# Performance work log

Measured on AMD Instinct MI355X. Metric: run time of the kernel, lower is better.

The kernel has to match this reference:

```python
import jax, jax.numpy as jnp
import numpy as np

N_NODES = 50000
N_REL = 8
D_IN = 64      # review_dim (in_feats)
D_OUT = 32     # attention_feats (final_dim)
H = 2          # num_heads
N_EDGES = 800000
NEG_SLOPE = 0.2


def gather_mm(x, w, b, idx):
    """Per-edge relation-indexed GEMM: out[e] = x[e] @ w[idx[e]] + b[idx[e]].
    Loops over the small fixed relation set (R=8) instead of materializing
    an [E, D, HF] gathered weight tensor."""
    out = jnp.zeros((x.shape[0], w.shape[-1]), dtype=x.dtype)
    for r in range(w.shape[0]):
        out = out + jnp.where((idx == r)[:, None], x @ w[r] + b[r], jnp.zeros((), x.dtype))
    return out


def setup_inputs() -> dict:
    key = jax.random.key(0)
    ks = jax.random.split(key, 11)
    feat = jax.random.normal(ks[0], (N_NODES, D_IN), dtype=jnp.float32)
    src = jax.random.randint(ks[1], (N_EDGES,), 0, N_NODES)
    dst = jax.random.randint(ks[2], (N_EDGES,), 0, N_NODES)
    r_type = jax.random.randint(ks[3], (N_EDGES,), 0, N_REL)
    nid = jax.random.randint(ks[4], (N_EDGES,), 0, N_NODES)
    fc_src = jax.random.normal(ks[5], (N_REL, D_IN, H * D_OUT), dtype=jnp.float32) * 0.1
    fc_src_bias = jax.random.normal(ks[6], (N_REL, H * D_OUT), dtype=jnp.float32) * 0.1
    node_quality = jax.random.normal(ks[7], (N_NODES, D_IN), dtype=jnp.float32)
    fc_qual = jax.random.normal(ks[8], (N_REL, D_IN, H * D_OUT), dtype=jnp.float32) * 0.1
    fc_qual_bias = jax.random.normal(ks[9], (N_REL, H * D_OUT), dtype=jnp.float32) * 0.1
    attn = jax.random.normal(ks[10], (N_REL, H, D_OUT), dtype=jnp.float32) * 0.1
    return {"feat": feat, "src": src, "dst": dst, "r_type": r_type, "nid": nid,
            "fc_src": fc_src, "fc_src_bias": fc_src_bias, "node_quality": node_quality,
            "fc_qual": fc_qual, "fc_qual_bias": fc_qual_bias, "attn": attn}


def reference(feat, src, dst, r_type, nid, fc_src, fc_src_bias,
              node_quality, fc_qual, fc_qual_bias, attn):
    E = src.shape[0]
    h_src = feat  # feat_drop is identity (p=0)

    # el: relation-aware projection of source features, per edge -> [E, H, D_OUT]
    el = gather_mm(h_src[src], fc_src, fc_src_bias, r_type).reshape(E, H, D_OUT)
    # qual: relation-aware projection of per-edge node-quality embedding
    h_qual = node_quality[nid]
    qual = gather_mm(h_qual, fc_qual, fc_qual_bias, r_type).reshape(E, H, D_OUT)

    # additive attention logits, relation-indexed attn vector -> [E, H]
    e = jax.nn.leaky_relu(el + qual, negative_slope=NEG_SLOPE)
    e = jnp.sum(e * attn[r_type], axis=-1)  # [E, H]

    # edge_softmax over incoming edges of each dst node (per head)
    emax = jax.ops.segment_max(e, dst, num_segments=N_NODES)  # [N, H]
    emax = jnp.where(jnp.isfinite(emax), emax, jnp.zeros((), e.dtype))
    ex = jnp.exp(e - emax[dst])
    denom = jax.ops.segment_sum(ex, dst, num_segments=N_NODES)
    a = ex / denom[dst]  # [E, H]

    # NARRE: messages are raw source features weighted by attention
    msg = h_src[src][:, None, :] * a[:, :, None]  # [E, H, D_IN]
    rst = jax.ops.segment_sum(msg, dst, num_segments=N_NODES)  # [N, H, D_IN]
    return rst
```

## Files before the change

kernel.cpp:

```cpp
#include <hip/hip_runtime.h>
#include <hip/hip_bf16.h>

#define NN 50000
#define NR 8
#define NE 800000
#define NBLK_E 3125
#define NWV (NBLK_E * 4)
#define NCH 13

typedef short bf16x8 __attribute__((ext_vector_type(8)));
typedef float f32x4  __attribute__((ext_vector_type(4)));

__device__ __forceinline__ unsigned fkey(float f) {
    unsigned b = __float_as_uint(f);
    return (b & 0x80000000u) ? ~b : (b | 0x80000000u);
}
__device__ __forceinline__ float funkey(unsigned k) {
    unsigned b = (k & 0x80000000u) ? (k ^ 0x80000000u) : ~k;
    return __uint_as_float(b);
}
__device__ __forceinline__ unsigned short f2bf(float f) {
    unsigned u = __float_as_uint(f);
    unsigned r = (u + 0x7FFFu + ((u >> 16) & 1u)) >> 16;
    return (unsigned short)r;
}
__device__ __forceinline__ float bf2f(unsigned short b) {
    return __uint_as_float(((unsigned)b) << 16);
}

__global__ __launch_bounds__(256) void conv_hist_kernel(
    const float* __restrict__ feat, const float* __restrict__ nq,
    const float* __restrict__ WS, const float* __restrict__ WQ,
    const float* __restrict__ bS, const float* __restrict__ bQ,
    const int* __restrict__ dst, const int* __restrict__ rt,
    unsigned short* __restrict__ xS, unsigned short* __restrict__ xQ,
    unsigned short* __restrict__ WtS, unsigned short* __restrict__ WtQ,
    float* __restrict__ bSQ,
    int* __restrict__ cnt, int* __restrict__ rank, int* __restrict__ rhist)
{
    const int t = threadIdx.x;
    const int idx = blockIdx.x * 256 + t;

    if (blockIdx.x < 2 * NBLK_E && (blockIdx.x & 1) == 0) {
        const int eb = blockIdx.x >> 1;
        const int e = eb * 256 + t;
        const int w = t >> 6, lane = t & 63;
        const int d = dst[e], r = rt[e];
        rank[e] = atomicAdd(&cnt[d], 1);
        #pragma unroll
        for (int rr = 0; rr < 8; ++rr) {
            const unsigned long long m = __ballot(r == rr);
            if (lane == 0) rhist[rr * NWV + eb * 4 + w] = __popcll(m);
        }
    }

    const int NX = NN * 64 / 4;
    if (idx < NX) {
        const float4 v = reinterpret_cast<const float4*>(feat)[idx];
        ushort4 p; p.x = f2bf(v.x); p.y = f2bf(v.y); p.z = f2bf(v.z); p.w = f2bf(v.w);
        reinterpret_cast<ushort4*>(xS)[idx] = p;
    } else if (idx < 2 * NX) {
        const float4 v = reinterpret_cast<const float4*>(nq)[idx - NX];
        ushort4 p; p.x = f2bf(v.x); p.y = f2bf(v.y); p.z = f2bf(v.z); p.w = f2bf(v.w);
        reinterpret_cast<ushort4*>(xQ)[idx - NX] = p;
    } else {
        int i = idx - 2 * NX;
        if (i < 32768) {
            const int r = i >> 12, rem = i & 4095, o = rem >> 6, k = rem & 63;
            WtS[i] = f2bf(WS[(size_t)r * 4096 + k * 64 + o]);
        } else if (i < 65536) {
            i -= 32768;
            const int r = i >> 12, rem = i & 4095, o = rem >> 6, k = rem & 63;
            WtQ[i] = f2bf(WQ[(size_t)r * 4096 + k * 64 + o]);
        } else if (i < 65536 + 512) {
            const int j = i - 65536;
            bSQ[j] = bS[j] + bQ[j];
        }
    }
}

__global__ __launch_bounds__(256) void scanrb1_kernel(
    const int* __restrict__ rhist, int* __restrict__ rbase0, int* __restrict__ psum)
{
    __shared__ int s[256];
    __shared__ int carry;
    const int c = blockIdx.x, r = blockIdx.y, t = threadIdx.x;
    if (t == 0) carry = 0;
    __syncthreads();
    const int i1 = min((c + 1) * 1024, NWV);
    for (int b0 = c * 1024; b0 < i1; b0 += 256) {
        const int i = b0 + t;
        const int v = (i < i1) ? rhist[r * NWV + i] : 0;
        s[t] = v;
        __syncthreads();
        #pragma unroll
        for (int off = 1; off < 256; off <<= 1) {
            const int x = (t >= off) ? s[t - off] : 0;
            __syncthreads();
            s[t] += x;
            __syncthreads();
        }
        if (i < i1) rbase0[r * NWV + i] = carry + s[t] - v;
        __syncthreads();
        if (t == 0) carry += s[255];
        __syncthreads();
    }
    if (t == 0) psum[r * NCH + c] = carry;
}

__global__ __launch_bounds__(256) void scan1_kernel(
    const int* __restrict__ cnt, int* __restrict__ offs, int* __restrict__ partial)
{
    __shared__ int s[256];
    const int t = threadIdx.x, i = blockIdx.x * 256 + t;
    const int v = (i < NN) ? cnt[i] : 0;
    s[t] = v;
    __syncthreads();
    #pragma unroll
    for (int off = 1; off < 256; off <<= 1) {
        const int x = (t >= off) ? s[t - off] : 0;
        __syncthreads();
        s[t] += x;
        __syncthreads();
    }
    if (i < NN) offs[i] = s[t] - v;
    if (t == 255) partial[blockIdx.x] = s[255];
}

__global__ __launch_bounds__(256) void scan2_kernel(
    int* __restrict__ partial, const int nblk,
    const int* __restrict__ psum, int* __restrict__ off_pad,
    int* __restrict__ cbase, int4* __restrict__ meta)
{
    __shared__ int s[256];
    __shared__ int sop[9];
    __shared__ int scr[8];
    const int t = threadIdx.x;
    const int v = (t < nblk) ? partial[t] : 0;
    s[t] = v;
    __syncthreads();
    #pragma unroll
    for (int off = 1; off < 256; off <<= 1) {
        const int x = (t >= off) ? s[t - off] : 0;
        __syncthreads();
        s[t] += x;
        __syncthreads();
    }
    if (t < nblk) partial[t] = s[t] - v;
    if (t == 0) {
        int cr[8];
        for (int r = 0; r < NR; ++r) {
            cr[r] = 0;
            for (int c = 0; c < NCH; ++c) cr[r] += psum[r * NCH + c];
        }
        int acc = 0;
        for (int r = 0; r < NR; ++r) {
            sop[r] = acc; off_pad[r] = acc; scr[r] = cr[r];
            int a2 = acc;
            for (int c = 0; c < NCH; ++c) { cbase[r * NCH + c] = a2; a2 += psum[r * NCH + c]; }
            acc += (cr[r] + 255) & ~255;
        }
        sop[8] = acc; off_pad[8] = acc;
    }
    __syncthreads();
    for (int r = 0; r < NR; ++r) {
        const int s0 = sop[r] + scr[r], s1 = sop[r + 1];
        for (int i = s0 + t; i < s1; i += 256) meta[i] = make_int4(0, 0, -1, 0);
    }
}

__global__ __launch_bounds__(256) void scan3_kernel(
    int* __restrict__ offs, const int* __restrict__ partial)
{
    const int i = blockIdx.x * 256 + threadIdx.x;
    if (i < NN) offs[i] += partial[blockIdx.x];
    if (i == 0) offs[NN] = NE;
}

__global__ __launch_bounds__(256) void fillr_kernel(
    const int* __restrict__ rt, const int* __restrict__ src,
    const int* __restrict__ nid, const int* __restrict__ dst,
    const int* __restrict__ offs, const int* __restrict__ rank,
    const int* __restrict__ rbase0, const int* __restrict__ cbase,
    int4* __restrict__ meta)
{
    const int t = threadIdx.x, e = blockIdx.x * 256 + t;
    const int w = t >> 6, lane = t & 63;
    const int r = rt[e];
    unsigned long long mymask = 0;
    #pragma unroll
    for (int rr = 0; rr < 8; ++rr) {
        const unsigned long long m = __ballot(r == rr);
        if (r == rr) mymask = m;
    }
    const int rk = (int)__popcll(mymask & ((1ull << lane) - 1ull));
    const int wv = blockIdx.x * 4 + w;
    const int slot = cbase[r * NCH + (wv >> 10)] + rbase0[r * NWV + wv] + rk;
    const int j = offs[dst[e]] + rank[e];
    meta[slot] = make_int4(src[e], nid[e], j, 0);
}

__global__ __launch_bounds__(256) void logits_kernel(
    const unsigned short* __restrict__ xS, const unsigned short* __restrict__ xQ,
    const unsigned short* __restrict__ WtS, const unsigned short* __restrict__ WtQ,
    const float* __restrict__ bSQ, const float* __restrict__ attn,
    const int4* __restrict__ meta, const int* __restrict__ off_pad,
    uint2* __restrict__ perm)
{
    __shared__ bf16x8 ldsS[512];
    __shared__ bf16x8 ldsQ[512];
    const int slot0 = blockIdx.x * 256;
    int r = 0;
    #pragma unroll
    for (int i = 1; i <= 8; ++i) r += (slot0 >= off_pad[i]);
    if (r >= 8) return;

    const int t = threadIdx.x;
    const int lane = t & 63, l15 = lane & 15, g = lane >> 4, l7 = l15 & 7;
    const int sbase = slot0 + (t >> 6) * 64;

    int4 mt[4];
    #pragma unroll
    for (int b = 0; b < 4; ++b) mt[b] = meta[sbase + b * 16 + l15];
    bf16x8 xf[4][2], qf[4][2];
    #pragma unroll
    for (int b = 0; b < 4; ++b) {
        const unsigned short* xp = xS + (size_t)mt[b].x * 64;
        const unsigned short* qp = xQ + (size_t)mt[b].y * 64;
        xf[b][0] = *reinterpret_cast<const bf16x8*>(xp + g * 8);
        xf[b][1] = *reinterpret_cast<const bf16x8*>(xp + 32 + g * 8);
        qf[b][0] = *reinterpret_cast<const bf16x8*>(qp + g * 8);
        qf[b][1] = *reinterpret_cast<const bf16x8*>(qp + 32 + g * 8);
    }

    #pragma unroll
    for (int i = 0; i < 2; ++i) {
        const int c = t + i * 256;
        const int row = c >> 3, c8 = c & 7, sw = c8 ^ (row & 7);
        ldsS[row * 8 + sw] = *reinterpret_cast<const bf16x8*>(WtS + (size_t)r * 4096 + c * 8);
        ldsQ[row * 8 + sw] = *reinterpret_cast<const bf16x8*>(WtQ + (size_t)r * 4096 + c * 8);
    }
    __syncthreads();

    float p0[4] = {0.f, 0.f, 0.f, 0.f}, p1[4] = {0.f, 0.f, 0.f, 0.f};
    #pragma unroll
    for (int ot = 0; ot < 4; ++ot) {
        const int row8 = (ot * 16 + l15) * 8;
        const bf16x8 wS0 = ldsS[row8 + (g ^ l7)];
        const bf16x8 wS1 = ldsS[row8 + ((4 + g) ^ l7)];
        const bf16x8 wQ0 = ldsQ[row8 + (g ^ l7)];
        const bf16x8 wQ1 = ldsQ[row8 + ((4 + g) ^ l7)];
        const f32x4 bv = *reinterpret_cast<const f32x4*>(bSQ  + r * 64 + ot * 16 + g * 4);
        const f32x4 av = *reinterpret_cast<const f32x4*>(attn + r * 64 + ot * 16 + g * 4);
        #pragma unroll
        for (int b = 0; b < 4; ++b) {
            f32x4 acc = (f32x4){0.f, 0.f, 0.f, 0.f};
            acc = __builtin_amdgcn_mfma_f32_16x16x32_bf16(wS0, xf[b][0], acc, 0, 0, 0);
            acc = __builtin_amdgcn_mfma_f32_16x16x32_bf16(wS1, xf[b][1], acc, 0, 0, 0);
            acc = __builtin_amdgcn_mfma_f32_16x16x32_bf16(wQ0, qf[b][0], acc, 0, 0, 0);
            acc = __builtin_amdgcn_mfma_f32_16x16x32_bf16(wQ1, qf[b][1], acc, 0, 0, 0);
            float part = 0.f;
            #pragma unroll
            for (int j = 0; j < 4; ++j) {
                float v = acc[j] + bv[j];
                v = v > 0.f ? v : 0.2f * v;
                part += v * av[j];
            }
            if (ot < 2) p0[b] += part; else p1[b] += part;
        }
    }
    #pragma unroll
    for (int b = 0; b < 4; ++b) {
        p0[b] += __shfl_xor(p0[b], 16); p0[b] += __shfl_xor(p0[b], 32);
        p1[b] += __shfl_xor(p1[b], 16); p1[b] += __shfl_xor(p1[b], 32);
        if (g == 0 && mt[b].z >= 0) {
            const unsigned pk = ((unsigned)f2bf(p0[b]) << 16) | (unsigned)f2bf(p1[b]);
            perm[mt[b].z] = make_uint2((unsigned)mt[b].x, pk);
        }
    }
}

__global__ __launch_bounds__(256) void aggregate_kernel(
    const unsigned short* __restrict__ xS, const int* __restrict__ offs,
    const uint2* __restrict__ perm, float* __restrict__ out)
{
    __shared__ float2 ebuf[4][64];
    __shared__ int    sbuf[4][64];
    const int wv = threadIdx.x >> 6;
    const int n = blockIdx.x * 4 + wv;
    if (n >= NN) return;
    const int lane = threadIdx.x & 63;
    const int h2 = lane >> 5;
    const int dp = lane & 31;
    const int s0 = offs[n], s1 = offs[n + 1];
    float a00 = 0.f, a01 = 0.f, a10 = 0.f, a11 = 0.f;
    float d0s = 0.f, d1s = 0.f;
    if (s1 > s0) {
        float m0 = -1e30f, m1 = -1e30f;
        for (int j = s0 + lane; j < s1; j += 64) {
            const uint2 p = perm[j];
            m0 = fmaxf(m0, bf2f((unsigned short)(p.y >> 16)));
            m1 = fmaxf(m1, bf2f((unsigned short)(p.y & 0xFFFFu)));
        }
        #pragma unroll
        for (int m = 32; m; m >>= 1) {
            m0 = fmaxf(m0, __shfl_xor(m0, m));
            m1 = fmaxf(m1, __shfl_xor(m1, m));
        }
        for (int c = s0; c < s1; c += 64) {
            const int cnt = min(64, s1 - c);
            if (lane < cnt) {
                const uint2 p = perm[c + lane];
                const float e0 = __expf(bf2f((unsigned short)(p.y >> 16)) - m0);
                const float e1 = __expf(bf2f((unsigned short)(p.y & 0xFFFFu)) - m1);
                d0s += e0; d1s += e1;
                ebuf[wv][lane] = make_float2(e0, e1);
                sbuf[wv][lane] = (int)p.x;
            } else if (lane == cnt) {
                ebuf[wv][lane] = make_float2(0.f, 0.f);
                sbuf[wv][lane] = 0;
            }
            const int cp = cnt + (cnt & 1);
            #pragma unroll 4
            for (int k = 0; k < cp; k += 2) {
                const int ei = k + h2;
                const int sA = sbuf[wv][ei];
                const float2 w = ebuf[wv][ei];
                const unsigned fv = *reinterpret_cast<const unsigned*>(
                    xS + (size_t)sA * 64 + dp * 2);
                const float fx = bf2f((unsigned short)(fv & 0xFFFFu));
                const float fy = bf2f((unsigned short)(fv >> 16));
                a00 += fx * w.x; a01 += fy * w.x;
                a10 += fx * w.y; a11 += fy * w.y;
            }
        }
        #pragma unroll
        for (int m = 32; m; m >>= 1) {
            d0s += __shfl_xor(d0s, m);
            d1s += __shfl_xor(d1s, m);
        }
        a00 += __shfl_xor(a00, 32); a01 += __shfl_xor(a01, 32);
        a10 += __shfl_xor(a10, 32); a11 += __shfl_xor(a11, 32);
        const float r0 = 1.f / d0s, r1 = 1.f / d1s;
        a00 *= r0; a01 *= r0; a10 *= r1; a11 *= r1;
    }
    if (h2 == 0)
        *reinterpret_cast<float2*>(&out[(size_t)n * 128 + dp * 2])      = make_float2(a00, a01);
    else
        *reinterpret_cast<float2*>(&out[(size_t)n * 128 + 64 + dp * 2]) = make_float2(a10, a11);
}

__global__ __launch_bounds__(256) void logits_direct_kernel(
    const float* __restrict__ feat, const float* __restrict__ nq,
    const int* __restrict__ src, const int* __restrict__ dst,
    const int* __restrict__ rt, const int* __restrict__ nid,
    const float* __restrict__ fc_src, const float* __restrict__ fc_src_b,
    const float* __restrict__ fc_qual, const float* __restrict__ fc_qual_b,
    const float* __restrict__ attn,
    float* __restrict__ e_buf, unsigned* __restrict__ emax)
{
    __shared__ float Ws[64][64];
    __shared__ float Wq[64][64];
    __shared__ float bl[64];
    __shared__ float al[64];
    const int r = blockIdx.y;
    const int t = threadIdx.x;
    for (int i = t; i < 4096; i += 256) {
        ((float*)Ws)[i] = fc_src[(size_t)r * 4096 + i];
        ((float*)Wq)[i] = fc_qual[(size_t)r * 4096 + i];
    }
    if (t < 64) {
        bl[t] = fc_src_b[r * 64 + t] + fc_qual_b[r * 64 + t];
        al[t] = attn[r * 64 + t];
    }
    __syncthreads();

    const int lane = t & 63;
    const int wid = blockIdx.x * 4 + (t >> 6);
    const int nw = gridDim.x * 4;
    for (int e = wid; e < NE; e += nw) {
        if (rt[e] != r) continue;
        const int s = src[e], q = nid[e];
        float fv = feat[(size_t)s * 64 + lane];
        float qv = nq[(size_t)q * 64 + lane];
        float acc = bl[lane];
        for (int k = 0; k < 64; ++k) {
            acc += __shfl(fv, k) * Ws[k][lane];
            acc += __shfl(qv, k) * Wq[k][lane];
        }
        acc = acc > 0.f ? acc : 0.2f * acc;
        float p = acc * al[lane];
        #pragma unroll
        for (int m = 1; m < 32; m <<= 1) p += __shfl_xor(p, m);
        if ((lane & 31) == 0) {
            int h = lane >> 5;
            e_buf[(size_t)e * 2 + h] = p;
            atomicMax(&emax[(size_t)dst[e] * 2 + h], fkey(p));
        }
    }
}

__global__ __launch_bounds__(256) void expdenom_kernel(
    const int* __restrict__ dst, float* __restrict__ e_buf,
    const unsigned* __restrict__ emax, float* __restrict__ denom)
{
    const int i = blockIdx.x * 256 + threadIdx.x;
    if (i >= NE * 2) return;
    const int e = i >> 1, h = i & 1;
    const int dn = dst[e];
    const float m = funkey(emax[(size_t)dn * 2 + h]);
    const float ex = __expf(e_buf[i] - m);
    e_buf[i] = ex;
    unsafeAtomicAdd(&denom[(size_t)dn * 2 + h], ex);
}

__global__ __launch_bounds__(256) void scatter_kernel(
    const float* __restrict__ feat, const int* __restrict__ src, const int* __restrict__ dst,
    const float* __restrict__ ex, const float* __restrict__ denom, float* __restrict__ out)
{
    const int e = blockIdx.x * 4 + (threadIdx.x >> 6);
    if (e >= NE) return;
    const int lane = threadIdx.x & 63;
    const int s = src[e], dn = dst[e];
    const float f = feat[(size_t)s * 64 + lane];
    const float a0 = ex[(size_t)e * 2]     / denom[(size_t)dn * 2];
    const float a1 = ex[(size_t)e * 2 + 1] / denom[(size_t)dn * 2 + 1];
    unsafeAtomicAdd(&out[(size_t)dn * 128 + lane],      f * a0);
    unsafeAtomicAdd(&out[(size_t)dn * 128 + 64 + lane], f * a1);
}

extern "C" void kernel_launch(void* const* d_in, const int* in_sizes, int n_in,
                              void* d_out, int out_size, void* d_ws, size_t ws_size,
                              hipStream_t stream)
{
    const float* feat      = (const float*)d_in[0];
    const int*   src       = (const int*)d_in[1];
    const int*   dst       = (const int*)d_in[2];
    const int*   rt        = (const int*)d_in[3];
    const int*   nid       = (const int*)d_in[4];
    const float* fc_src    = (const float*)d_in[5];
    const float* fc_src_b  = (const float*)d_in[6];
    const float* nq        = (const float*)d_in[7];
    const float* fc_qual   = (const float*)d_in[8];
    const float* fc_qual_b = (const float*)d_in[9];
    const float* attn      = (const float*)d_in[10];
    float* out = (float*)d_out;

    char* ws = (char*)d_ws;

    int*    cnt      = (int*)ws;
    int*    offs     = (int*)(ws + 262144);
    int*    partial  = (int*)(ws + 524288);
    int*    off_pad  = (int*)(ws + 528384);
    int*    psum     = (int*)(ws + 528512);
    int*    cbase    = (int*)(ws + 528960);
    int*    rhist    = (int*)(ws + 655360);
    int*    rbase0   = (int*)(ws + 1055360);
    int*    rank     = (int*)(ws + 1455360);
    int4*   meta     = (int4*)(ws + 4718592);
    uint2*  perm     = (uint2*)(ws + 17551360);
    unsigned short* xS  = (unsigned short*)(ws + 30351360);
    unsigned short* xQ  = (unsigned short*)(ws + 36751360);
    unsigned short* WtS = (unsigned short*)(ws + 43151360);
    unsigned short* WtQ = (unsigned short*)(ws + 43216896);
    float*          bSQ = (float*)(ws + 43282432);
    const size_t need = 43284480;

    if (ws_size >= need) {
        hipMemsetAsync(cnt, 0, 200000, stream);

        conv_hist_kernel<<<6508, 256, 0, stream>>>(
            feat, nq, fc_src, fc_qual, fc_src_b, fc_qual_b, dst, rt,
            xS, xQ, WtS, WtQ, bSQ, cnt, rank, rhist);
        {
            dim3 g(NCH, NR);
            scanrb1_kernel<<<g, 256, 0, stream>>>(rhist, rbase0, psum);
        }

        const int nblk = (NN + 255) / 256;
        scan1_kernel<<<nblk, 256, 0, stream>>>(cnt, offs, partial);
        scan2_kernel<<<1, 256, 0, stream>>>(partial, nblk, psum, off_pad, cbase, meta);
        scan3_kernel<<<nblk, 256, 0, stream>>>(offs, partial);
        fillr_kernel<<<NBLK_E, 256, 0, stream>>>(
            rt, src, nid, dst, offs, rank, rbase0, cbase, meta);

        logits_kernel<<<(NE + 8 * 256) / 256, 256, 0, stream>>>(
            xS, xQ, WtS, WtQ, bSQ, attn, meta, off_pad, perm);
        aggregate_kernel<<<(NN + 3) / 4, 256, 0, stream>>>(xS, offs, perm, out);
    } else {
        float*    e_buf = (float*)ws;
        unsigned* emax  = (unsigned*)(ws + (size_t)NE * 2 * 4);
        float*    denom = (float*)(ws + (size_t)NE * 2 * 4 + (size_t)NN * 2 * 4);
        hipMemsetAsync(out, 0, (size_t)out_size * sizeof(float), stream);
        hipMemsetAsync(emax, 0, (size_t)NN * 2 * 4 * 2, stream);
        dim3 g(256, NR);
        logits_direct_kernel<<<g, 256, 0, stream>>>(
            feat, nq, src, dst, rt, nid, fc_src, fc_src_b, fc_qual, fc_qual_b,
            attn, e_buf, emax);
        expdenom_kernel<<<(NE * 2 + 255) / 256, 256, 0, stream>>>(dst, e_buf, emax, denom);
        scatter_kernel<<<(NE + 3) / 4, 256, 0, stream>>>(feat, src, dst, e_buf, denom, out);
    }
}
```

Measured before the change: 146.0 us.

## Merge scan kernels, make logits kernel persistent, use shuffles in aggregate

Fuses the node-count scan and the per-relation histogram scan into one launch to drop a kernel launch. Turns the logits kernel into a grid-stride persistent kernel over 1024 blocks, so a block reloads the relation weights into shared memory only when the relation changes. Replaces the shared-memory staging of edge weights and source ids in aggregate with wave shuffles. The persistent loop gives up some parallelism and adds barriers whenever the relation changes.

```diff
diff --git a/kernel.cpp b/kernel.cpp
--- a/kernel.cpp
+++ b/kernel.cpp
@@ -7,6 +7,8 @@
 #define NBLK_E 3125
 #define NWV (NBLK_E * 4)
 #define NCH 13
+#define NBLK_SCAN1 196
+#define LOGITS_BLOCKS 1024
 
 typedef short bf16x8 __attribute__((ext_vector_type(8)));
 typedef float f32x4  __attribute__((ext_vector_type(4)));
@@ -79,18 +81,16 @@
     }
 }
 
-__global__ __launch_bounds__(256) void scanrb1_kernel(
+__global__ __launch_bounds__(256) void scan1rb_kernel(
+    const int* __restrict__ cnt, int* __restrict__ offs, int* __restrict__ partial,
     const int* __restrict__ rhist, int* __restrict__ rbase0, int* __restrict__ psum)
 {
     __shared__ int s[256];
     __shared__ int carry;
-    const int c = blockIdx.x, r = blockIdx.y, t = threadIdx.x;
-    if (t == 0) carry = 0;
-    __syncthreads();
-    const int i1 = min((c + 1) * 1024, NWV);
-    for (int b0 = c * 1024; b0 < i1; b0 += 256) {
-        const int i = b0 + t;
-        const int v = (i < i1) ? rhist[r * NWV + i] : 0;
+    const int t = threadIdx.x;
+    if (blockIdx.x < NBLK_SCAN1) {
+        const int i = blockIdx.x * 256 + t;
+        const int v = (i < NN) ? cnt[i] : 0;
         s[t] = v;
         __syncthreads();
         #pragma unroll
@@ -100,31 +100,33 @@
             s[t] += x;
             __syncthreads();
         }
-        if (i < i1) rbase0[r * NWV + i] = carry + s[t] - v;
+        if (i < NN) offs[i] = s[t] - v;
+        if (t == 255) partial[blockIdx.x] = s[255];
+    } else {
+        const int bb = blockIdx.x - NBLK_SCAN1;
+        const int c = bb % NCH, r = bb / NCH;
+        if (t == 0) carry = 0;
         __syncthreads();
-        if (t == 0) carry += s[255];
-        __syncthreads();
-    }
-    if (t == 0) psum[r * NCH + c] = carry;
-}
-
-__global__ __launch_bounds__(256) void scan1_kernel(
-    const int* __restrict__ cnt, int* __restrict__ offs, int* __restrict__ partial)
-{
-    __shared__ int s[256];
-    const int t = threadIdx.x, i = blockIdx.x * 256 + t;
-    const int v = (i < NN) ? cnt[i] : 0;
-    s[t] = v;
-    __syncthreads();
-    #pragma unroll
-    for (int off = 1; off < 256; off <<= 1) {
-        const int x = (t >= off) ? s[t - off] : 0;
-        __syncthreads();
-        s[t] += x;
-        __syncthreads();
-    }
-    if (i < NN) offs[i] = s[t] - v;
-    if (t == 255) partial[blockIdx.x] = s[255];
+        const int i1 = min((c + 1) * 1024, NWV);
+        for (int b0 = c * 1024; b0 < i1; b0 += 256) {
+            const int i = b0 + t;
+            const int v = (i < i1) ? rhist[r * NWV + i] : 0;
+            s[t] = v;
+            __syncthreads();
+            #pragma unroll
+            for (int off = 1; off < 256; off <<= 1) {
+                const int x = (t >= off) ? s[t - off] : 0;
+                __syncthreads();
+                s[t] += x;
+                __syncthreads();
+            }
+            if (i < i1) rbase0[r * NWV + i] = carry + s[t] - v;
+            __syncthreads();
+            if (t == 0) carry += s[255];
+            __syncthreads();
+        }
+        if (t == 0) psum[r * NCH + c] = carry;
+    }
 }
 
 __global__ __launch_bounds__(256) void scan2_kernel(
@@ -209,73 +211,80 @@
 {
     __shared__ bf16x8 ldsS[512];
     __shared__ bf16x8 ldsQ[512];
-    const int slot0 = blockIdx.x * 256;
-    int r = 0;
-    #pragma unroll
-    for (int i = 1; i <= 8; ++i) r += (slot0 >= off_pad[i]);
-    if (r >= 8) return;
-
     const int t = threadIdx.x;
     const int lane = t & 63, l15 = lane & 15, g = lane >> 4, l7 = l15 & 7;
-    const int sbase = slot0 + (t >> 6) * 64;
-
-    int4 mt[4];
-    #pragma unroll
-    for (int b = 0; b < 4; ++b) mt[b] = meta[sbase + b * 16 + l15];
-    bf16x8 xf[4][2], qf[4][2];
-    #pragma unroll
-    for (int b = 0; b < 4; ++b) {
-        const unsigned short* xp = xS + (size_t)mt[b].x * 64;
-        const unsigned short* qp = xQ + (size_t)mt[b].y * 64;
-        xf[b][0] = *reinterpret_cast<const bf16x8*>(xp + g * 8);
-        xf[b][1] = *reinterpret_cast<const bf16x8*>(xp + 32 + g * 8);
-        qf[b][0] = *reinterpret_cast<const bf16x8*>(qp + g * 8);
-        qf[b][1] = *reinterpret_cast<const bf16x8*>(qp + 32 + g * 8);
-    }
-
-    #pragma unroll
-    for (int i = 0; i < 2; ++i) {
-        const int c = t + i * 256;
-        const int row = c >> 3, c8 = c & 7, sw = c8 ^ (row & 7);
-        ldsS[row * 8 + sw] = *reinterpret_cast<const bf16x8*>(WtS + (size_t)r * 4096 + c * 8);
-        ldsQ[row * 8 + sw] = *reinterpret_cast<const bf16x8*>(WtQ + (size_t)r * 4096 + c * 8);
-    }
-    __syncthreads();
-
-    float p0[4] = {0.f, 0.f, 0.f, 0.f}, p1[4] = {0.f, 0.f, 0.f, 0.f};
-    #pragma unroll
-    for (int ot = 0; ot < 4; ++ot) {
-        const int row8 = (ot * 16 + l15) * 8;
-        const bf16x8 wS0 = ldsS[row8 + (g ^ l7)];
-        const bf16x8 wS1 = ldsS[row8 + ((4 + g) ^ l7)];
-        const bf16x8 wQ0 = ldsQ[row8 + (g ^ l7)];
-        const bf16x8 wQ1 = ldsQ[row8 + ((4 + g) ^ l7)];
-        const f32x4 bv = *reinterpret_cast<const f32x4*>(bSQ  + r * 64 + ot * 16 + g * 4);
-        const f32x4 av = *reinterpret_cast<const f32x4*>(attn + r * 64 + ot * 16 + g * 4);
+    const int ntile = off_pad[8] >> 8;
+
+    int r_cur = -1;
+    for (int tile = blockIdx.x; tile < ntile; tile += LOGITS_BLOCKS) {
+        const int slot0 = tile * 256;
+        int r = 0;
+        #pragma unroll
+        for (int i = 1; i <= 8; ++i) r += (slot0 >= off_pad[i]);
+
+        const int sbase = slot0 + (t >> 6) * 64;
+        int4 mt[4];
+        #pragma unroll
+        for (int b = 0; b < 4; ++b) mt[b] = meta[sbase + b * 16 + l15];
+        bf16x8 xf[4][2], qf[4][2];
         #pragma unroll
         for (int b = 0; b < 4; ++b) {
-            f32x4 acc = (f32x4){0.f, 0.f, 0.f, 0.f};
-            acc = __builtin_amdgcn_mfma_f32_16x16x32_bf16(wS0, xf[b][0], acc, 0, 0, 0);
-            acc = __builtin_amdgcn_mfma_f32_16x16x32_bf16(wS1, xf[b][1], acc, 0, 0, 0);
-            acc = __builtin_amdgcn_mfma_f32_16x16x32_bf16(wQ0, qf[b][0], acc, 0, 0, 0);
-            acc = __builtin_amdgcn_mfma_f32_16x16x32_bf16(wQ1, qf[b][1], acc, 0, 0, 0);
-            float part = 0.f;
+            const unsigned short* xp = xS + (size_t)mt[b].x * 64;
+            const unsigned short* qp = xQ + (size_t)mt[b].y * 64;
+            xf[b][0] = *reinterpret_cast<const bf16x8*>(xp + g * 8);
+            xf[b][1] = *reinterpret_cast<const bf16x8*>(xp + 32 + g * 8);
+            qf[b][0] = *reinterpret_cast<const bf16x8*>(qp + g * 8);
+            qf[b][1] = *reinterpret_cast<const bf16x8*>(qp + 32 + g * 8);
+        }
+
+        if (r != r_cur) {
+            if (r_cur >= 0) __syncthreads();
             #pragma unroll
-            for (int j = 0; j < 4; ++j) {
-                float v = acc[j] + bv[j];
-                v = v > 0.f ? v : 0.2f * v;
-                part += v * av[j];
+            for (int i = 0; i < 2; ++i) {
+                const int c = t + i * 256;
+                const int row = c >> 3, c8 = c & 7, sw = c8 ^ (row & 7);
+                ldsS[row * 8 + sw] = *reinterpret_cast<const bf16x8*>(WtS + (size_t)r * 4096 + c * 8);
+                ldsQ[row * 8 + sw] = *reinterpret_cast<const bf16x8*>(WtQ + (size_t)r * 4096 + c * 8);
             }
-            if (ot < 2) p0[b] += part; else p1[b] += part;
-        }
-    }
-    #pragma unroll
-    for (int b = 0; b < 4; ++b) {
-        p0[b] += __shfl_xor(p0[b], 16); p0[b] += __shfl_xor(p0[b], 32);
-        p1[b] += __shfl_xor(p1[b], 16); p1[b] += __shfl_xor(p1[b], 32);
-        if (g == 0 && mt[b].z >= 0) {
-            const unsigned pk = ((unsigned)f2bf(p0[b]) << 16) | (unsigned)f2bf(p1[b]);
-            perm[mt[b].z] = make_uint2((unsigned)mt[b].x, pk);
+            __syncthreads();
+            r_cur = r;
+        }
+
+        float p0[4] = {0.f, 0.f, 0.f, 0.f}, p1[4] = {0.f, 0.f, 0.f, 0.f};
+        #pragma unroll
+        for (int ot = 0; ot < 4; ++ot) {
+            const int row8 = (ot * 16 + l15) * 8;
+            const bf16x8 wS0 = ldsS[row8 + (g ^ l7)];
+            const bf16x8 wS1 = ldsS[row8 + ((4 + g) ^ l7)];
+            const bf16x8 wQ0 = ldsQ[row8 + (g ^ l7)];
+            const bf16x8 wQ1 = ldsQ[row8 + ((4 + g) ^ l7)];
+            const f32x4 bv = *reinterpret_cast<const f32x4*>(bSQ  + r * 64 + ot * 16 + g * 4);
+            const f32x4 av = *reinterpret_cast<const f32x4*>(attn + r * 64 + ot * 16 + g * 4);
+            #pragma unroll
+            for (int b = 0; b < 4; ++b) {
+                f32x4 acc = (f32x4){0.f, 0.f, 0.f, 0.f};
+                acc = __builtin_amdgcn_mfma_f32_16x16x32_bf16(wS0, xf[b][0], acc, 0, 0, 0);
+                acc = __builtin_amdgcn_mfma_f32_16x16x32_bf16(wS1, xf[b][1], acc, 0, 0, 0);
+                acc = __builtin_amdgcn_mfma_f32_16x16x32_bf16(wQ0, qf[b][0], acc, 0, 0, 0);
+                acc = __builtin_amdgcn_mfma_f32_16x16x32_bf16(wQ1, qf[b][1], acc, 0, 0, 0);
+                float part = 0.f;
+                #pragma unroll
+                for (int j = 0; j < 4; ++j) {
+                    float v = acc[j] + bv[j];
+                    v = v > 0.f ? v : 0.2f * v;
+                    part += v * av[j];
+                }
+                if (ot < 2) p0[b] += part; else p1[b] += part;
+            }
+        }
+        #pragma unroll
+        for (int b = 0; b < 4; ++b) {
+            p0[b] += __shfl_xor(p0[b], 16); p0[b] += __shfl_xor(p0[b], 32);
+            p1[b] += __shfl_xor(p1[b], 16); p1[b] += __shfl_xor(p1[b], 32);
+            if (g == 0 && mt[b].z >= 0) {
+                const unsigned pk = ((unsigned)f2bf(p0[b]) << 16) | (unsigned)f2bf(p1[b]);
+                perm[mt[b].z] = make_uint2((unsigned)mt[b].x, pk);
+            }
         }
     }
 }
@@ -284,8 +293,6 @@
     const unsigned short* __restrict__ xS, const int* __restrict__ offs,
     const uint2* __restrict__ perm, float* __restrict__ out)
 {
-    __shared__ float2 ebuf[4][64];
-    __shared__ int    sbuf[4][64];
     const int wv = threadIdx.x >> 6;
     const int n = blockIdx.x * 4 + wv;
     if (n >= NN) return;
@@ -309,29 +316,27 @@
         }
         for (int c = s0; c < s1; c += 64) {
             const int cnt = min(64, s1 - c);
+            int esrc = 0; float e0 = 0.f, e1 = 0.f;
             if (lane < cnt) {
                 const uint2 p = perm[c + lane];
-                const float e0 = __expf(bf2f((unsigned short)(p.y >> 16)) - m0);
-                const float e1 = __expf(bf2f((unsigned short)(p.y & 0xFFFFu)) - m1);
+                e0 = __expf(bf2f((unsigned short)(p.y >> 16)) - m0);
+                e1 = __expf(bf2f((unsigned short)(p.y & 0xFFFFu)) - m1);
                 d0s += e0; d1s += e1;
-                ebuf[wv][lane] = make_float2(e0, e1);
-                sbuf[wv][lane] = (int)p.x;
-            } else if (lane == cnt) {
-                ebuf[wv][lane] = make_float2(0.f, 0.f);
-                sbuf[wv][lane] = 0;
+                esrc = (int)p.x;
             }
             const int cp = cnt + (cnt & 1);
             #pragma unroll 4
             for (int k = 0; k < cp; k += 2) {
                 const int ei = k + h2;
-                const int sA = sbuf[wv][ei];
-                const float2 w = ebuf[wv][ei];
+                const int sA = __shfl(esrc, ei);
+                const float w0 = __shfl(e0, ei);
+                const float w1 = __shfl(e1, ei);
                 const unsigned fv = *reinterpret_cast<const unsigned*>(
                     xS + (size_t)sA * 64 + dp * 2);
                 const float fx = bf2f((unsigned short)(fv & 0xFFFFu));
                 const float fy = bf2f((unsigned short)(fv >> 16));
-                a00 += fx * w.x; a01 += fy * w.x;
-                a10 += fx * w.y; a11 += fy * w.y;
+                a00 += fx * w0; a01 += fy * w0;
+                a10 += fx * w1; a11 += fy * w1;
             }
         }
         #pragma unroll
@@ -472,19 +477,15 @@
         conv_hist_kernel<<<6508, 256, 0, stream>>>(
             feat, nq, fc_src, fc_qual, fc_src_b, fc_qual_b, dst, rt,
             xS, xQ, WtS, WtQ, bSQ, cnt, rank, rhist);
-        {
-            dim3 g(NCH, NR);
-            scanrb1_kernel<<<g, 256, 0, stream>>>(rhist, rbase0, psum);
-        }
-
-        const int nblk = (NN + 255) / 256;
-        scan1_kernel<<<nblk, 256, 0, stream>>>(cnt, offs, partial);
-        scan2_kernel<<<1, 256, 0, stream>>>(partial, nblk, psum, off_pad, cbase, meta);
-        scan3_kernel<<<nblk, 256, 0, stream>>>(offs, partial);
+
+        scan1rb_kernel<<<NBLK_SCAN1 + NCH * NR, 256, 0, stream>>>(
+            cnt, offs, partial, rhist, rbase0, psum);
+        scan2_kernel<<<1, 256, 0, stream>>>(partial, NBLK_SCAN1, psum, off_pad, cbase, meta);
+        scan3_kernel<<<NBLK_SCAN1, 256, 0, stream>>>(offs, partial);
         fillr_kernel<<<NBLK_E, 256, 0, stream>>>(
             rt, src, nid, dst, offs, rank, rbase0, cbase, meta);
 
-        logits_kernel<<<(NE + 8 * 256) / 256, 256, 0, stream>>>(
+        logits_kernel<<<LOGITS_BLOCKS, 256, 0, stream>>>(
             xS, xQ, WtS, WtQ, bSQ, attn, meta, off_pad, perm);
         aggregate_kernel<<<(NN + 3) / 4, 256, 0, stream>>>(xS, offs, perm, out);
     } else {
```

Result: slower. 157.8 us (+8.1%).
